# Optimization experiments

Measured on AMD Instinct MI355X. Metric: run time of the kernel, lower is better.

The kernel has to match this reference:

```python
import jax, jax.numpy as jnp
import numpy as np

BS, S, D, N, E = 16, 8, 10, 32, 300
H, STATE_DIM, MID, OC = 128, 96, 256, 100

def setup_inputs():
    ks = jax.random.split(jax.random.key(0), 24)
    g = lambda i, shape: (0.02 * jax.random.normal(ks[i], shape)).astype(jnp.float32)
    return {
        "stock_news": jax.random.normal(ks[0], (BS, S, D, N, E), dtype=jnp.float32),
        "stock_feats": jax.random.normal(ks[1], (BS, STATE_DIM), dtype=jnp.float32),
        "conv_w3": g(2, (S, OC, E, 3)), "conv_b3": g(3, (S, OC)),
        "conv_w4": g(4, (S, OC, E, 4)), "conv_b4": g(5, (S, OC)),
        "conv_w5": g(6, (S, OC, E, 5)), "conv_b5": g(7, (S, OC)),
        "w_ih": g(8, (S, 4 * H, 3 * OC)), "w_hh": g(9, (S, 4 * H, H)),
        "b_ih": g(10, (S, 4 * H)), "b_hh": g(11, (S, 4 * H)),
        "linX_w": g(12, (S, H, 2 * H)), "linX_b": g(13, (S, H)),
        "linY_w": g(14, (S, 64, H)), "linY_b": g(15, (S, 64)),
        "w1": g(16, (24, STATE_DIM)), "b1": g(17, (24,)),
        "w2": g(18, (16, 24)), "b2": g(19, (16,)),
        "arch_w1": g(20, (MID, 16 + 64 * S)), "arch_b1": g(21, (MID,)),
        "arch_w2": g(22, (S, MID)), "arch_b2": g(23, (S,)),
        "action_var": jnp.full((S,), -0.25, dtype=jnp.float32),
    }

def _conv_maxpool(x, w, b, k):
    # x: [S,B,D,N,E], w: [S,OC,E,k] -> conv1d over news axis then max-pool -> [S,B,D,OC]
    L = x.shape[3] - k + 1
    y = jnp.broadcast_to(b[:, None, None, None, :], (x.shape[0], x.shape[1], x.shape[2], L, w.shape[1]))
    for j in range(k):
        y = y + jnp.einsum('sbdne,soe->sbdno', x[:, :, :, j:j + L, :], w[:, :, :, j])
    return y.max(axis=3)

def _lstm_attn(xs, w_ih, w_hh, b_ih, b_hh):
    # single-stock LSTM (batch_first) + attention from original code; xs: [B,D,I] -> [B,2H]
    pre = jnp.einsum('bdi,gi->dbg', xs, w_ih) + b_ih + b_hh  # [D,B,4H]
    h0 = jnp.zeros((xs.shape[0], w_hh.shape[1]), xs.dtype)
    def step(carry, g_t):
        h, c = carry
        gates = g_t + h @ w_hh.T
        i, f, g, o = jnp.split(gates, 4, axis=-1)  # PyTorch gate order i,f,g,o
        c = jax.nn.sigmoid(f) * c + jax.nn.sigmoid(i) * jnp.tanh(g)
        h = jax.nn.sigmoid(o) * jnp.tanh(c)
        return (h, c), h
    (hn, _), outs = jax.lax.scan(step, (h0, h0), pre)
    outs = outs.transpose(1, 0, 2)  # [B,D,H]
    w = jnp.einsum('bh,bdh->bd', hn, outs)[:, None, :]  # [B,1,D]
    w = jax.nn.softmax(w, axis=1)  # softmax over singleton dim, exactly as torch code (yields ones)
    out = jnp.sum(w.transpose(0, 2, 1) * outs, axis=1)  # [B,H]
    return jnp.concatenate([hn, out], axis=-1)  # [B,2H]

def _forward(stock_news, stock_feats, conv_w3, conv_b3, conv_w4, conv_b4, conv_w5, conv_b5,
             w_ih, w_hh, b_ih, b_hh, linX_w, linX_b, linY_w, linY_b,
             w1, b1, w2, b2, arch_w1, arch_b1, arch_w2, arch_b2, action_var):
    x = stock_news.transpose(1, 0, 2, 3, 4)  # [S,B,D,N,E]
    feats = [_conv_maxpool(x, w, b, k) for (w, b, k) in
             ((conv_w3, conv_b3, 3), (conv_w4, conv_b4, 4), (conv_w5, conv_b5, 5))]
    text = jnp.concatenate(feats, axis=-1)  # [S,B,D,300]
    comb = jax.vmap(_lstm_attn)(text, w_ih, w_hh, b_ih, b_hh)  # [S,B,2H]
    hX = jax.nn.relu(jnp.einsum('sbi,shi->sbh', comb, linX_w) + linX_b[:, None, :])  # dropout is eval-mode identity
    hY = jax.nn.relu(jnp.einsum('sbh,soh->sbo', hX, linY_w) + linY_b[:, None, :])  # [S,B,64]
    stock_text = hY.transpose(1, 0, 2).reshape(stock_news.shape[0], -1)  # [B,S*64]
    f = jax.nn.relu(stock_feats @ w1.T + b1) @ w2.T + b2  # [B,16]
    total = jnp.concatenate([stock_text, f], axis=-1)  # [B,16+64S]
    mu = jnp.tanh(jax.nn.relu(total @ arch_w1.T + arch_b1) @ arch_w2.T + arch_b2)
    return mu, jnp.exp(action_var)

def reference(stock_news, stock_feats, conv_w3, conv_b3, conv_w4, conv_b4, conv_w5, conv_b5,
              w_ih, w_hh, b_ih, b_hh, linX_w, linX_b, linY_w, linY_b,
              w1, b1, w2, b2, arch_w1, arch_b1, arch_w2, arch_b2, action_var):
    return _forward(stock_news, stock_feats, conv_w3, conv_b3, conv_w4, conv_b4, conv_w5, conv_b5,
                    w_ih, w_hh, b_ih, b_hh, linX_w, linX_b, linY_w, linY_b,
                    w1, b1, w2, b2, arch_w1, arch_b1, arch_w2, arch_b2, action_var)
```

## Files before the change

kernel.cpp:

```cpp
#include <hip/hip_runtime.h>
#include <math.h>

#define S_   8
#define B_   16
#define D_   10
#define N_   32
#define E_   300
#define H_   128
#define G4_  512
#define SDIM_ 96
#define MID_ 256
#define TOT_ 528

#define NWPACK 3850240
#define NWPRE  1310720

typedef unsigned short u16;
typedef __attribute__((ext_vector_type(8))) short short8;
typedef __attribute__((ext_vector_type(4))) short short4v;
typedef __attribute__((ext_vector_type(4))) float f32x4;

static __device__ __forceinline__ u16 f2bf(float f) {
    unsigned u = __builtin_bit_cast(unsigned, f);
    return (u16)((u + 0x7FFFu + ((u >> 16) & 1u)) >> 16);
}

__global__ void prep(const float* __restrict__ w3, const float* __restrict__ b3,
                     const float* __restrict__ w4, const float* __restrict__ b4,
                     const float* __restrict__ w5, const float* __restrict__ b5,
                     const float* __restrict__ w_ih,
                     const float* __restrict__ lxw, const float* __restrict__ lyw,
                     const float* __restrict__ aw1,
                     u16* __restrict__ wpack2, u16* __restrict__ wpre2,
                     float* __restrict__ bcomb,
                     float* __restrict__ lxwT, float* __restrict__ lywT,
                     float* __restrict__ aw1T) {
    int idx = blockIdx.x * blockDim.x + threadIdx.x;
    if (idx < NWPACK) {
        int j = idx & 7, q = (idx >> 3) & 3;
        int rest = idx >> 5;
        int c = rest % 320, ks = (rest / 320) % 47, s = rest / 15040;
        int kk = ks * 32 + q * 8 + j;
        int tap = kk / 300, e = kk - tap * 300;
        float v = 0.f;
        if (tap < 5) {
            if (c < 100)      { if (tap < 3) v = w3[((s*100 + c      )*300 + e)*3 + tap]; }
            else if (c < 200) { if (tap < 4) v = w4[((s*100 + c - 100)*300 + e)*4 + tap]; }
            else if (c < 300) {              v = w5[((s*100 + c - 200)*300 + e)*5 + tap]; }
        }
        wpack2[idx] = f2bf(v);
    } else if (idx < NWPACK + NWPRE) {
        int i2 = idx - NWPACK;
        int j = i2 & 7, q = (i2 >> 3) & 3;
        int rest = i2 >> 5;
        int g = rest & 511, ks = (rest >> 9) % 10, s = rest / 5120;
        int kk = ks * 32 + q * 8 + j;
        float v = (kk < 300) ? w_ih[((size_t)s * 512 + g) * 300 + kk] : 0.f;
        wpre2[i2] = f2bf(v);
    }
    if (idx < 262144) {
        int t = idx & 127, i = (idx >> 7) & 255, s = idx >> 15;
        lxwT[idx] = lxw[((size_t)(s * 128 + t)) * 256 + i];
    }
    if (idx < 65536) {
        int t = idx & 63, i = (idx >> 6) & 127, s = idx >> 13;
        lywT[idx] = lyw[((size_t)(s * 64 + t)) * 128 + i];
    }
    if (idx < 135168) {
        int j = idx & 255, i = idx >> 8;
        aw1T[idx] = aw1[(size_t)j * TOT_ + i];
    }
    if (idx < 2560) {
        int c = idx % 320, s = idx / 320;
        float bv = 0.f;
        if (c < 100)      bv = b3[s*100 + c];
        else if (c < 200) bv = b4[s*100 + c - 100];
        else if (c < 300) bv = b5[s*100 + c - 200];
        bcomb[idx] = bv;
    }
}

__global__ __launch_bounds__(512, 2) void conv_mfma(const float* __restrict__ news,
                                                    const u16* __restrict__ wpack2,
                                                    const float* __restrict__ bcomb,
                                                    u16* __restrict__ text_bf) {
    __shared__ u16 xs[5 * 10816];
    __shared__ float part[10][320];
    const int tid = threadIdx.x, bid = blockIdx.x;
    const int s = bid & 7, rr_ = bid >> 3, b = rr_ >> 1, half = rr_ & 1;
    const int l = tid & 63, wvi = tid >> 6;
    const int wm = wvi >> 2, wn = wvi & 3;
    const int q = l >> 4, r16 = l & 15;

    const u16* gp[5];
#pragma unroll
    for (int nt = 0; nt < 5; ++nt) {
        int c = wn * 80 + nt * 16 + r16;
        gp[nt] = wpack2 + (size_t)s * 481280 + c * 32 + q * 8;
    }

    short8 bf0[5], bf1[5];
#pragma unroll
    for (int nt = 0; nt < 5; ++nt) bf0[nt] = *reinterpret_cast<const short8*>(gp[nt]);
#pragma unroll
    for (int nt = 0; nt < 5; ++nt) bf1[nt] = *reinterpret_cast<const short8*>(gp[nt] + 10240);

    for (int day = 0; day < 5; ++day) {
        const float4* xg = reinterpret_cast<const float4*>(
            news + (size_t)((b * 8 + s) * 10 + half * 5 + day) * 9600);
        for (int i = tid; i < 2704; i += 512) {
            ushort4 u;
            if (i < 2400) {
                float4 v = xg[i];
                u.x = f2bf(v.x); u.y = f2bf(v.y); u.z = f2bf(v.z); u.w = f2bf(v.w);
            } else { u.x = 0; u.y = 0; u.z = 0; u.w = 0; }
            *reinterpret_cast<ushort4*>(&xs[day * 10816 + 4 * i]) = u;
        }
    }
    __syncthreads();

    f32x4 acc[5][5];
#pragma unroll
    for (int mt = 0; mt < 5; ++mt)
#pragma unroll
        for (int nt = 0; nt < 5; ++nt) acc[mt][nt] = (f32x4)(0.f);

#define LOADA(dst, ks) do {                                                       \
    _Pragma("unroll")                                                             \
    for (int mt_ = 0; mt_ < 5; ++mt_) {                                           \
        int di_ = wm * 5 + mt_;                                                   \
        int off_ = (di_ >> 1) * 10816 + (((di_ & 1) << 4) + r16) * 300            \
                   + (ks) * 32 + q * 8;                                           \
        short4v lo_ = *reinterpret_cast<const short4v*>(&xs[off_]);               \
        short4v hi_ = *reinterpret_cast<const short4v*>(&xs[off_ + 4]);           \
        dst[mt_] = __builtin_shufflevector(lo_, hi_, 0, 1, 2, 3, 4, 5, 6, 7);     \
    } } while (0)

#define MFMAS(bfv, av) do {                                                       \
    __builtin_amdgcn_s_setprio(1);                                                \
    _Pragma("unroll")                                                             \
    for (int nt_ = 0; nt_ < 5; ++nt_)                                             \
        _Pragma("unroll")                                                         \
        for (int mt_ = 0; mt_ < 5; ++mt_)                                         \
            acc[mt_][nt_] = __builtin_amdgcn_mfma_f32_16x16x32_bf16(av[mt_], bfv[nt_], acc[mt_][nt_], 0, 0, 0); \
    __builtin_amdgcn_s_setprio(0);                                                \
    } while (0)

    for (int ks = 0; ks < 46; ks += 2) {
        short8 a0[5], a1[5];
        LOADA(a0, ks);
        MFMAS(bf0, a0);
#pragma unroll
        for (int nt = 0; nt < 5; ++nt)
            bf0[nt] = *reinterpret_cast<const short8*>(gp[nt] + (ks + 2) * 10240);

        LOADA(a1, ks + 1);
        MFMAS(bf1, a1);
        if (ks + 3 < 47) {
#pragma unroll
            for (int nt = 0; nt < 5; ++nt)
                bf1[nt] = *reinterpret_cast<const short8*>(gp[nt] + (ks + 3) * 10240);
        }
    }
    {
        short8 a0[5];
        LOADA(a0, 46);
        MFMAS(bf0, a0);
    }
#undef LOADA
#undef MFMAS

#pragma unroll
    for (int mt = 0; mt < 5; ++mt) {
        const int di = wm * 5 + mt;
        const int nwb = (di & 1) << 4;
#pragma unroll
        for (int nt = 0; nt < 5; ++nt) {
            int oc = wn * 80 + nt * 16 + r16;
            int L = (oc < 100) ? 30 : (oc < 200) ? 29 : 28;
            float mx = -3e38f;
#pragma unroll
            for (int rr = 0; rr < 4; ++rr) {
                int nw = nwb + q * 4 + rr;
                if (nw < L) mx = fmaxf(mx, acc[mt][nt][rr]);
            }
            mx = fmaxf(mx, __shfl_xor(mx, 16));
            mx = fmaxf(mx, __shfl_xor(mx, 32));
            if (l < 16) part[di][wn * 80 + nt * 16 + l] = mx;
        }
    }
    __syncthreads();
    for (int i = tid; i < 1600; i += 512) {
        int day = i / 320, oc = i - day * 320;
        float mx = fmaxf(part[2 * day][oc], part[2 * day + 1][oc]);
        text_bf[((size_t)(s * 16 + b) * 10 + half * 5 + day) * 320 + oc] =
            f2bf(mx + bcomb[s * 320 + oc]);
    }
}

__global__ __launch_bounds__(256) void lstm_pre_mfma(const u16* __restrict__ text_bf,
                                                     const u16* __restrict__ wpre2,
                                                     const float* __restrict__ b_ih,
                                                     const float* __restrict__ b_hh,
                                                     float* __restrict__ pre) {
    __shared__ u16 as16[16 * 320];
    const int sd = blockIdx.x, s = sd / 10, d = sd % 10;
    const int tid = threadIdx.x, l = tid & 63, w = tid >> 6, q = l >> 4, r16 = l & 15;

    for (int i = tid; i < 640; i += 256) {
        int r = i / 40, c = i % 40;
        *reinterpret_cast<float4*>(as16 + r * 320 + ((c ^ (r & 7)) << 3)) =
            *reinterpret_cast<const float4*>(text_bf + ((size_t)(s * 16 + r) * 10 + d) * 320 + c * 8);
    }
    __syncthreads();

    const u16* gpb[8];
#pragma unroll
    for (int nt = 0; nt < 8; ++nt) {
        int g = w * 128 + nt * 16 + r16;
        gpb[nt] = wpre2 + (size_t)s * 163840 + g * 32 + q * 8;
    }

    f32x4 acc[8];
#pragma unroll
    for (int nt = 0; nt < 8; ++nt) acc[nt] = (f32x4)(0.f);

    for (int ks = 0; ks < 10; ++ks) {
        short8 a = *reinterpret_cast<const short8*>(
            as16 + r16 * 320 + (((ks * 4 + q) ^ (r16 & 7)) << 3));
#pragma unroll
        for (int nt = 0; nt < 8; ++nt) {
            short8 bf = *reinterpret_cast<const short8*>(gpb[nt] + ks * 16384);
            acc[nt] = __builtin_amdgcn_mfma_f32_16x16x32_bf16(a, bf, acc[nt], 0, 0, 0);
        }
    }

#pragma unroll
    for (int nt = 0; nt < 8; ++nt) {
        int g = w * 128 + nt * 16 + r16;
        float bias = b_ih[s * 512 + g] + b_hh[s * 512 + g];
#pragma unroll
        for (int r = 0; r < 4; ++r) {
            int brow = q * 4 + r;
            pre[((size_t)sd * 16 + brow) * 512 + g] = acc[nt][r] + bias;
        }
    }
}

__global__ __launch_bounds__(512) void lstm_tail(const float* __restrict__ pre,
                                                 const float* __restrict__ w_hh,
                                                 const float* __restrict__ lxwT, const float* __restrict__ lxb,
                                                 const float* __restrict__ lywT, const float* __restrict__ lyb,
                                                 float* __restrict__ total) {
    __shared__ float wchunk[128][129];
    __shared__ float h_lds[H_];
    __shared__ float gates[G4_];
    __shared__ float comb_l[256];
    __shared__ __align__(16) float hx[H_];
    const int sb = blockIdx.x;
    const int s = sb / B_, b = sb % B_;
    const int t = threadIdx.x;

    float wrs[128];
    for (int c = 0; c < 4; ++c) {
        for (int i2 = t; i2 < 128 * 32; i2 += 512) {
            int row = i2 >> 5, fq = i2 & 31;
            float4 v = *reinterpret_cast<const float4*>(
                w_hh + ((size_t)(s * G4_ + c * 128 + row)) * H_ + fq * 4);
            wchunk[row][fq * 4 + 0] = v.x; wchunk[row][fq * 4 + 1] = v.y;
            wchunk[row][fq * 4 + 2] = v.z; wchunk[row][fq * 4 + 3] = v.w;
        }
        __syncthreads();
        if ((t >> 7) == c) {
            int r = t & 127;
#pragma unroll
            for (int i = 0; i < 128; ++i) wrs[i] = wchunk[r][i];
        }
        __syncthreads();
    }

    float cc = 0.f, hsum = 0.f, hval = 0.f;
    if (t < H_) h_lds[t] = 0.f;
    __syncthreads();

    for (int d = 0; d < D_; ++d) {
        float a0 = pre[(((size_t)(s * D_ + d) * B_ + b)) * G4_ + t];
        float a1 = 0.f, a2 = 0.f, a3 = 0.f;
#pragma unroll
        for (int i = 0; i < 128; i += 4) {
            float4 h4 = *reinterpret_cast<const float4*>(&h_lds[i]);
            a0 = fmaf(wrs[i + 0], h4.x, a0);
            a1 = fmaf(wrs[i + 1], h4.y, a1);
            a2 = fmaf(wrs[i + 2], h4.z, a2);
            a3 = fmaf(wrs[i + 3], h4.w, a3);
        }
        gates[t] = (a0 + a1) + (a2 + a3);
        __syncthreads();
        if (t < H_) {
            float ig = 1.f / (1.f + expf(-gates[t]));
            float fg = 1.f / (1.f + expf(-gates[H_ + t]));
            float gg = tanhf(gates[2 * H_ + t]);
            float og = 1.f / (1.f + expf(-gates[3 * H_ + t]));
            cc = fg * cc + ig * gg;
            hval = og * tanhf(cc);
            hsum += hval;
            h_lds[t] = hval;
        }
        __syncthreads();
    }
    if (t < H_) { comb_l[t] = hval; comb_l[H_ + t] = hsum; }
    __syncthreads();
    if (t < H_) {
        const float* wv = lxwT + (size_t)s * 256 * 128 + t;
        float a0 = lxb[s * H_ + t], a1 = 0.f;
        for (int i = 0; i < 256; i += 2) {
            a0 = fmaf(comb_l[i], wv[(size_t)i * 128], a0);
            a1 = fmaf(comb_l[i + 1], wv[(size_t)(i + 1) * 128], a1);
        }
        hx[t] = fmaxf(a0 + a1, 0.f);
    }
    __syncthreads();
    if (t < 64) {
        const float* wv = lywT + (size_t)s * 128 * 64 + t;
        float a0 = lyb[s * 64 + t], a1 = 0.f;
        for (int i = 0; i < 128; i += 2) {
            a0 = fmaf(hx[i], wv[(size_t)i * 64], a0);
            a1 = fmaf(hx[i + 1], wv[(size_t)(i + 1) * 64], a1);
        }
        total[(size_t)b * 512 + s * 64 + t] = fmaxf(a0 + a1, 0.f);
    }
}

__global__ __launch_bounds__(512) void head_feats(const float* __restrict__ total,
                                                  const float* __restrict__ sf,
                                                  const float* __restrict__ w1, const float* __restrict__ b1,
                                                  const float* __restrict__ w2, const float* __restrict__ b2,
                                                  const float* __restrict__ aw1T, const float* __restrict__ ab1,
                                                  const float* __restrict__ aw2, const float* __restrict__ ab2,
                                                  const float* __restrict__ avar,
                                                  float* __restrict__ out) {
    __shared__ __align__(16) float tr[TOT_];
    __shared__ float hid[MID_];
    __shared__ float h1f[24];
    __shared__ float pA[MID_], pB[MID_];
    const int bb = blockIdx.x, t = threadIdx.x;
    if (t < 128)
        reinterpret_cast<float4*>(tr)[t] = reinterpret_cast<const float4*>(total + (size_t)bb * 512)[t];
    if (t < 24) {
        float acc = b1[t];
        for (int i = 0; i < SDIM_; ++i) acc = fmaf(sf[bb * SDIM_ + i], w1[t * SDIM_ + i], acc);
        h1f[t] = fmaxf(acc, 0.f);
    }
    __syncthreads();
    if (t < 16) {
        float acc = b2[t];
        for (int i = 0; i < 24; ++i) acc = fmaf(h1f[i], w2[t * 24 + i], acc);
        tr[512 + t] = acc;
    }
    __syncthreads();
    {
        const int j = t & 255, hf = t >> 8;
        const int ilo = hf ? 264 : 0, ihi = hf ? 528 : 264;
        const float* wv = aw1T + j;
        float a0 = 0.f, a1 = 0.f, a2 = 0.f, a3 = 0.f;
        for (int i = ilo; i < ihi; i += 4) {
            a0 = fmaf(tr[i + 0], wv[(size_t)(i + 0) * 256], a0);
            a1 = fmaf(tr[i + 1], wv[(size_t)(i + 1) * 256], a1);
            a2 = fmaf(tr[i + 2], wv[(size_t)(i + 2) * 256], a2);
            a3 = fmaf(tr[i + 3], wv[(size_t)(i + 3) * 256], a3);
        }
        float p = (a0 + a1) + (a2 + a3);
        if (hf) pB[j] = p; else pA[j] = p;
    }
    __syncthreads();
    if (t < MID_) hid[t] = fmaxf(pA[t] + pB[t] + ab1[t], 0.f);
    __syncthreads();
    if (t < 8) {
        float acc = ab2[t];
        const float* wv = aw2 + (size_t)t * MID_;
        for (int i = 0; i < MID_; ++i) acc = fmaf(hid[i], wv[i], acc);
        out[bb * 8 + t] = tanhf(acc);
    }
    if (bb == 0 && t >= 8 && t < 16) out[128 + (t - 8)] = expf(avar[t - 8]);
}

extern "C" void kernel_launch(void* const* d_in, const int* in_sizes, int n_in,
                              void* d_out, int out_size, void* d_ws, size_t ws_size,
                              hipStream_t stream) {
    const float* news = (const float*)d_in[0];
    const float* sf   = (const float*)d_in[1];
    const float* w3   = (const float*)d_in[2];  const float* b3 = (const float*)d_in[3];
    const float* w4   = (const float*)d_in[4];  const float* b4 = (const float*)d_in[5];
    const float* w5   = (const float*)d_in[6];  const float* b5 = (const float*)d_in[7];
    const float* w_ih = (const float*)d_in[8];  const float* w_hh = (const float*)d_in[9];
    const float* b_ih = (const float*)d_in[10]; const float* b_hh = (const float*)d_in[11];
    const float* lxw  = (const float*)d_in[12]; const float* lxb = (const float*)d_in[13];
    const float* lyw  = (const float*)d_in[14]; const float* lyb = (const float*)d_in[15];
    const float* w1   = (const float*)d_in[16]; const float* b1 = (const float*)d_in[17];
    const float* w2   = (const float*)d_in[18]; const float* b2 = (const float*)d_in[19];
    const float* aw1  = (const float*)d_in[20]; const float* ab1 = (const float*)d_in[21];
    const float* aw2  = (const float*)d_in[22]; const float* ab2 = (const float*)d_in[23];
    const float* avar = (const float*)d_in[24];

    char* ws = (char*)d_ws;
    u16*   wpack2  = (u16*)ws;
    u16*   wpre2   = (u16*)(ws + 7700480);
    float* bcomb   = (float*)(ws + 10321920);
    u16*   text_bf = (u16*)(ws + 10332160);
    float* pre     = (float*)(ws + 11151360);
    float* total   = (float*)(ws + 13772800);
    float* lxwT    = (float*)(ws + 13805568);
    float* lywT    = (float*)(ws + 14854144);
    float* aw1T    = (float*)(ws + 15116288);

    prep<<<(NWPACK + NWPRE + 255) / 256, 256, 0, stream>>>(w3, b3, w4, b4, w5, b5, w_ih,
                                                           lxw, lyw, aw1,
                                                           wpack2, wpre2, bcomb, lxwT, lywT, aw1T);
    conv_mfma<<<256, 512, 0, stream>>>(news, wpack2, bcomb, text_bf);
    lstm_pre_mfma<<<S_ * D_, 256, 0, stream>>>(text_bf, wpre2, b_ih, b_hh, pre);
    lstm_tail<<<S_ * B_, 512, 0, stream>>>(pre, w_hh, lxwT, lxb, lywT, lyb, total);
    head_feats<<<B_, 512, 0, stream>>>(total, sf, w1, b1, w2, b2, aw1T, ab1, aw2, ab2, avar, (float*)d_out);
}
```

Measured before the change: 135.8 us.

## Vectorize weight packing, batch news staging loads, relax conv occupancy and priority

The prep kernel becomes a grid-stride loop in which each thread packs eight bf16 weights and writes them with vector stores, launched on a fixed 1024-block grid. The conv kernel now stages all five days of news with eight independent float4 loads in flight per thread before converting, and zero-fills the padding separately. It also drops the s_setprio calls around the MFMA block and changes launch_bounds minimum blocks from 2 to 1, giving the compiler more registers. The goals are fewer tiny stores, more memory-level parallelism and less register pressure, at the cost of possible occupancy loss.

```diff
diff --git a/kernel.cpp b/kernel.cpp
--- a/kernel.cpp
+++ b/kernel.cpp
@@ -15,6 +15,13 @@
 #define NWPACK 3850240
 #define NWPRE  1310720
 
+#define U_WPACK  481280
+#define U_WPRE   645120
+#define U_LXWT   907264
+#define U_LYWT   972800
+#define U_AW1T   1107968
+#define U_BCOMB  1110528
+
 typedef unsigned short u16;
 typedef __attribute__((ext_vector_type(8))) short short8;
 typedef __attribute__((ext_vector_type(4))) short short4v;
@@ -35,52 +42,66 @@
                      float* __restrict__ bcomb,
                      float* __restrict__ lxwT, float* __restrict__ lywT,
                      float* __restrict__ aw1T) {
-    int idx = blockIdx.x * blockDim.x + threadIdx.x;
-    if (idx < NWPACK) {
-        int j = idx & 7, q = (idx >> 3) & 3;
-        int rest = idx >> 5;
-        int c = rest % 320, ks = (rest / 320) % 47, s = rest / 15040;
-        int kk = ks * 32 + q * 8 + j;
-        int tap = kk / 300, e = kk - tap * 300;
-        float v = 0.f;
-        if (tap < 5) {
-            if (c < 100)      { if (tap < 3) v = w3[((s*100 + c      )*300 + e)*3 + tap]; }
-            else if (c < 200) { if (tap < 4) v = w4[((s*100 + c - 100)*300 + e)*4 + tap]; }
-            else if (c < 300) {              v = w5[((s*100 + c - 200)*300 + e)*5 + tap]; }
-        }
-        wpack2[idx] = f2bf(v);
-    } else if (idx < NWPACK + NWPRE) {
-        int i2 = idx - NWPACK;
-        int j = i2 & 7, q = (i2 >> 3) & 3;
-        int rest = i2 >> 5;
-        int g = rest & 511, ks = (rest >> 9) % 10, s = rest / 5120;
-        int kk = ks * 32 + q * 8 + j;
-        float v = (kk < 300) ? w_ih[((size_t)s * 512 + g) * 300 + kk] : 0.f;
-        wpre2[i2] = f2bf(v);
-    }
-    if (idx < 262144) {
-        int t = idx & 127, i = (idx >> 7) & 255, s = idx >> 15;
-        lxwT[idx] = lxw[((size_t)(s * 128 + t)) * 256 + i];
-    }
-    if (idx < 65536) {
-        int t = idx & 63, i = (idx >> 6) & 127, s = idx >> 13;
-        lywT[idx] = lyw[((size_t)(s * 64 + t)) * 128 + i];
-    }
-    if (idx < 135168) {
-        int j = idx & 255, i = idx >> 8;
-        aw1T[idx] = aw1[(size_t)j * TOT_ + i];
-    }
-    if (idx < 2560) {
-        int c = idx % 320, s = idx / 320;
-        float bv = 0.f;
-        if (c < 100)      bv = b3[s*100 + c];
-        else if (c < 200) bv = b4[s*100 + c - 100];
-        else if (c < 300) bv = b5[s*100 + c - 200];
-        bcomb[idx] = bv;
-    }
-}
-
-__global__ __launch_bounds__(512, 2) void conv_mfma(const float* __restrict__ news,
+    const int stride = gridDim.x * blockDim.x;
+    for (int u = blockIdx.x * blockDim.x + threadIdx.x; u < U_BCOMB; u += stride) {
+        if (u < U_WPACK) {
+            int q = u & 3, t = u >> 2;
+            int c = t % 320, t2 = t / 320;
+            int ks = t2 % 47, s = t2 / 47;
+            u16 o[8];
+#pragma unroll
+            for (int j = 0; j < 8; ++j) {
+                int kk = ks * 32 + q * 8 + j;
+                int tap = kk / 300, e = kk - tap * 300;
+                float v = 0.f;
+                if (tap < 5) {
+                    if (c < 100)      { if (tap < 3) v = w3[((s*100 + c      )*300 + e)*3 + tap]; }
+                    else if (c < 200) { if (tap < 4) v = w4[((s*100 + c - 100)*300 + e)*4 + tap]; }
+                    else if (c < 300) {              v = w5[((s*100 + c - 200)*300 + e)*5 + tap]; }
+                }
+                o[j] = f2bf(v);
+            }
+            *reinterpret_cast<ushort4*>(&wpack2[u * 8])     = make_ushort4(o[0], o[1], o[2], o[3]);
+            *reinterpret_cast<ushort4*>(&wpack2[u * 8 + 4]) = make_ushort4(o[4], o[5], o[6], o[7]);
+        } else if (u < U_WPRE) {
+            int u2 = u - U_WPACK;
+            int q = u2 & 3, t = u2 >> 2;
+            int g = t & 511, t2 = t >> 9;
+            int ks = t2 % 10, s = t2 / 10;
+            u16 o[8];
+#pragma unroll
+            for (int j = 0; j < 8; ++j) {
+                int kk = ks * 32 + q * 8 + j;
+                float v = (kk < 300) ? w_ih[((size_t)s * 512 + g) * 300 + kk] : 0.f;
+                o[j] = f2bf(v);
+            }
+            *reinterpret_cast<ushort4*>(&wpre2[u2 * 8])     = make_ushort4(o[0], o[1], o[2], o[3]);
+            *reinterpret_cast<ushort4*>(&wpre2[u2 * 8 + 4]) = make_ushort4(o[4], o[5], o[6], o[7]);
+        } else if (u < U_LXWT) {
+            int i = u - U_WPRE;
+            int t = i & 127, ii = (i >> 7) & 255, s = i >> 15;
+            lxwT[i] = lxw[((size_t)(s * 128 + t)) * 256 + ii];
+        } else if (u < U_LYWT) {
+            int i = u - U_LXWT;
+            int t = i & 63, ii = (i >> 6) & 127, s = i >> 13;
+            lywT[i] = lyw[((size_t)(s * 64 + t)) * 128 + ii];
+        } else if (u < U_AW1T) {
+            int i = u - U_LYWT;
+            int j = i & 255, ii = i >> 8;
+            aw1T[i] = aw1[(size_t)j * TOT_ + ii];
+        } else {
+            int i = u - U_AW1T;
+            int c = i % 320, s = i / 320;
+            float bv = 0.f;
+            if (c < 100)      bv = b3[s*100 + c];
+            else if (c < 200) bv = b4[s*100 + c - 100];
+            else if (c < 300) bv = b5[s*100 + c - 200];
+            bcomb[i] = bv;
+        }
+    }
+}
+
+__global__ __launch_bounds__(512, 1) void conv_mfma(const float* __restrict__ news,
                                                     const u16* __restrict__ wpack2,
                                                     const float* __restrict__ bcomb,
                                                     u16* __restrict__ text_bf) {
@@ -105,16 +126,31 @@
 #pragma unroll
     for (int nt = 0; nt < 5; ++nt) bf1[nt] = *reinterpret_cast<const short8*>(gp[nt] + 10240);
 
-    for (int day = 0; day < 5; ++day) {
+    {
         const float4* xg = reinterpret_cast<const float4*>(
-            news + (size_t)((b * 8 + s) * 10 + half * 5 + day) * 9600);
-        for (int i = tid; i < 2704; i += 512) {
-            ushort4 u;
-            if (i < 2400) {
-                float4 v = xg[i];
-                u.x = f2bf(v.x); u.y = f2bf(v.y); u.z = f2bf(v.z); u.w = f2bf(v.w);
-            } else { u.x = 0; u.y = 0; u.z = 0; u.w = 0; }
-            *reinterpret_cast<ushort4*>(&xs[day * 10816 + 4 * i]) = u;
+            news + (size_t)((b * 8 + s) * 10 + half * 5) * 9600);
+        for (int base = 0; base < 12000; base += 4096) {
+            float4 v[8];
+#pragma unroll
+            for (int j = 0; j < 8; ++j) {
+                int idx = base + j * 512 + tid;
+                if (idx < 12000) v[j] = xg[idx];
+            }
+#pragma unroll
+            for (int j = 0; j < 8; ++j) {
+                int idx = base + j * 512 + tid;
+                if (idx < 12000) {
+                    int day = idx / 2400, rem = idx - day * 2400;
+                    ushort4 o;
+                    o.x = f2bf(v[j].x); o.y = f2bf(v[j].y);
+                    o.z = f2bf(v[j].z); o.w = f2bf(v[j].w);
+                    *reinterpret_cast<ushort4*>(&xs[day * 10816 + rem * 4]) = o;
+                }
+            }
+        }
+        for (int i = tid; i < 1520; i += 512) {
+            int day = i / 304, p = i - day * 304;
+            *reinterpret_cast<unsigned*>(&xs[day * 10816 + 9600 + p * 2]) = 0u;
         }
     }
     __syncthreads();
@@ -137,13 +173,11 @@
     } } while (0)
 
 #define MFMAS(bfv, av) do {                                                       \
-    __builtin_amdgcn_s_setprio(1);                                                \
     _Pragma("unroll")                                                             \
     for (int nt_ = 0; nt_ < 5; ++nt_)                                             \
         _Pragma("unroll")                                                         \
         for (int mt_ = 0; mt_ < 5; ++mt_)                                         \
             acc[mt_][nt_] = __builtin_amdgcn_mfma_f32_16x16x32_bf16(av[mt_], bfv[nt_], acc[mt_][nt_], 0, 0, 0); \
-    __builtin_amdgcn_s_setprio(0);                                                \
     } while (0)
 
     for (int ks = 0; ks < 46; ks += 2) {
@@ -413,9 +447,8 @@
     float* lywT    = (float*)(ws + 14854144);
     float* aw1T    = (float*)(ws + 15116288);
 
-    prep<<<(NWPACK + NWPRE + 255) / 256, 256, 0, stream>>>(w3, b3, w4, b4, w5, b5, w_ih,
-                                                           lxw, lyw, aw1,
-                                                           wpack2, wpre2, bcomb, lxwT, lywT, aw1T);
+    prep<<<1024, 256, 0, stream>>>(w3, b3, w4, b4, w5, b5, w_ih, lxw, lyw, aw1,
+                                   wpack2, wpre2, bcomb, lxwT, lywT, aw1T);
     conv_mfma<<<256, 512, 0, stream>>>(news, wpack2, bcomb, text_bf);
     lstm_pre_mfma<<<S_ * D_, 256, 0, stream>>>(text_bf, wpre2, b_ih, b_hh, pre);
     lstm_tail<<<S_ * B_, 512, 0, stream>>>(pre, w_hh, lxwT, lxb, lywT, lyb, total);
```

Measured after the change: 142.4 us. +4.8%, slower.
